# Kernel optimization log

Measured on AMD Instinct MI355X. Metric: run time of the kernel, lower is better.

The kernel has to match this reference:

```python
import jax, jax.numpy as jnp
import numpy as np

NUM_HEADS = 8
NUM_POINTS = 4


def _bilinear(img, xs, ys):
    """Bilinear sample with zero padding (grid_sample align_corners=False).
    img: [N, H, W, C]; xs, ys: [N, P] pixel-space coords. Returns [N, P, C]."""
    H, W = img.shape[1], img.shape[2]
    x0 = jnp.floor(xs)
    y0 = jnp.floor(ys)
    wx = xs - x0
    wy = ys - y0
    x0i = x0.astype(jnp.int32)
    y0i = y0.astype(jnp.int32)

    def g(ix, iy):
        valid = ((ix >= 0) & (ix < W) & (iy >= 0) & (iy < H)).astype(img.dtype)
        ixc = jnp.clip(ix, 0, W - 1)
        iyc = jnp.clip(iy, 0, H - 1)
        v = jax.vmap(lambda im, yy, xx: im[yy, xx])(img, iyc, ixc)  # [N,P,C]
        return v * valid[..., None]

    return (g(x0i, y0i) * ((1 - wx) * (1 - wy))[..., None]
            + g(x0i + 1, y0i) * (wx * (1 - wy))[..., None]
            + g(x0i, y0i + 1) * ((1 - wx) * wy)[..., None]
            + g(x0i + 1, y0i + 1) * (wx * wy)[..., None])


def setup_inputs() -> dict:
    key = jax.random.key(0)
    ks = jax.random.split(key, 10)
    BN, C, H, W = 12, 256, 40, 100
    nq = H * W
    hp = NUM_HEADS * NUM_POINTS
    s = 1.0 / np.sqrt(C).astype(np.float32)
    return {
        "img_feats": jax.random.normal(ks[0], (BN, C, H, W), jnp.float32),
        "warp_grid": jax.random.uniform(ks[1], (BN, H, W, 2), jnp.float32),
        "reference_points": jax.random.uniform(ks[2], (BN, nq, 1, 2), jnp.float32),
        "Wv": jax.random.normal(ks[3], (C, C), jnp.float32) * s,
        "bv": jnp.zeros((C,), jnp.float32),
        "Woff": jax.random.normal(ks[4], (C, hp * 2), jnp.float32) * 0.01,
        "boff": jax.random.normal(ks[5], (hp * 2,), jnp.float32) * 0.5,
        "Wattn": jax.random.normal(ks[6], (C, hp), jnp.float32) * 0.01,
        "battn": jnp.zeros((hp,), jnp.float32),
        "Wout": jax.random.normal(ks[7], (C, C), jnp.float32) * s,
        "bout": jnp.zeros((C,), jnp.float32),
    }


def reference(img_feats, warp_grid, reference_points,
              Wv, bv, Woff, boff, Wattn, battn, Wout, bout):
    BN, C, H, W = img_feats.shape
    heads, pts = NUM_HEADS, NUM_POINTS
    hd = C // heads
    nq = H * W

    feat = img_feats.transpose(0, 2, 3, 1)  # [BN, H, W, C]

    # BEVWarp: bilinear warp of image features at the projected grid ([0,1] normed)
    gx = warp_grid[..., 0].reshape(BN, -1) * W - 0.5
    gy = warp_grid[..., 1].reshape(BN, -1) * H - 0.5
    warped = _bilinear(feat, gx, gy)          # [BN, nq, C] -> value
    query = feat.reshape(BN, nq, C)           # flattened img feats -> query

    # MultiScaleDeformableAttention, num_levels=1
    v = (warped @ Wv + bv).reshape(BN, nq, heads, hd)
    off = (query @ Woff + boff).reshape(BN, nq, heads, pts, 2)
    attn = jax.nn.softmax((query @ Wattn + battn).reshape(BN, nq, heads, pts), axis=-1)

    norm = jnp.array([W, H], dtype=img_feats.dtype)
    loc = reference_points.reshape(BN, nq, 1, 1, 2) + off / norm  # [BN,nq,h,p,2]

    vh = v.transpose(0, 2, 1, 3).reshape(BN * heads, H, W, hd)
    lx = (loc[..., 0] * W - 0.5).transpose(0, 2, 1, 3).reshape(BN * heads, nq * pts)
    ly = (loc[..., 1] * H - 0.5).transpose(0, 2, 1, 3).reshape(BN * heads, nq * pts)
    sampled = _bilinear(vh, lx, ly).reshape(BN, heads, nq, pts, hd)

    agg = jnp.einsum('bhqpd,bqhp->bqhd', sampled, attn).reshape(BN, nq, C)
    out = agg @ Wout + bout + query  # output_proj + residual (dropout=0 at eval)
    return out.transpose(0, 2, 1).reshape(BN, C, H, W)
```

## Files before the change

### kernel.cpp

```cpp
#include <hip/hip_runtime.h>

#define DEVINL __device__ __forceinline__

typedef __attribute__((ext_vector_type(4))) float f32x4;
typedef __attribute__((ext_vector_type(8))) short short8;

constexpr int kBN = 12, kC = 256, kH = 40, kW = 100;
constexpr int kNQ = kH * kW;
constexpr int kM = kBN * kNQ;

DEVINL float bflo(uint p) { union { uint i; float f; } v; v.i = p << 16; return v.f; }
DEVINL float bfhi(uint p) { union { uint i; float f; } v; v.i = p & 0xffff0000u; return v.f; }
DEVINL ushort f2bf(float f) {
  union { float f; uint i; } v; v.f = f;
  uint i = v.i;
  return (ushort)((i + 0x7fffu + ((i >> 16) & 1u)) >> 16);
}
DEVINL uint pack2(float a, float b) { return (uint)f2bf(a) | ((uint)f2bf(b) << 16); }

DEVINL void mfma_bf16(f32x4& acc, short8 a, short8 b) {
  acc = __builtin_amdgcn_mfma_f32_16x16x32_bf16(a, b, acc, 0, 0, 0);
}

DEVINL void acc8(float* acc, uint4 d, float wv) {
  acc[0] += wv * bflo(d.x); acc[1] += wv * bfhi(d.x);
  acc[2] += wv * bflo(d.y); acc[3] += wv * bfhi(d.y);
  acc[4] += wv * bflo(d.z); acc[5] += wv * bfhi(d.z);
  acc[6] += wv * bflo(d.w); acc[7] += wv * bfhi(d.w);
}

__global__ __launch_bounds__(256) void k_wt(const float* __restrict__ W,
                                            ushort* __restrict__ WT, int K, int N) {
  int idx = blockIdx.x * 256 + threadIdx.x;
  if (idx >= K * N) return;
  int n = idx / K, k = idx - n * K;
  WT[idx] = f2bf(W[k * N + n]);
}

__global__ __launch_bounds__(256) void k_transpose(const float* __restrict__ img,
                                                   ushort* __restrict__ feat) {
  __shared__ ushort tile[64][66];
  int b = blockIdx.z, c0 = blockIdx.y * 64, q0 = blockIdx.x * 64;
  int t = threadIdx.x;
  int ql = t & 63, cl = t >> 6;
#pragma unroll
  for (int i = 0; i < 16; ++i) {
    int c = cl + i * 4, q = q0 + ql;
    float v = (q < kNQ) ? img[(size_t)(b * kC + c0 + c) * kNQ + q] : 0.f;
    tile[c][ql] = f2bf(v);
  }
  __syncthreads();
  int cc = t & 63, qr = t >> 6;
#pragma unroll
  for (int i = 0; i < 16; ++i) {
    int qlo = qr + i * 4, q = q0 + qlo;
    if (q < kNQ) feat[(size_t)(b * kNQ + q) * kC + c0 + cc] = tile[cc][qlo];
  }
}

__global__ __launch_bounds__(256) void k_warp(const ushort* __restrict__ feat,
                                              const float* __restrict__ grid,
                                              ushort* __restrict__ warped) {
  int orig = blockIdx.x;
  int n = (orig & 7) * 750 + (orig >> 3);
  int t = threadIdx.x;
  int ql = t >> 5, g = t & 31;
  int gq = n * 8 + ql;
  int b = gq / kNQ, q = gq - b * kNQ;
  float gx = grid[(size_t)gq * 2 + 0] * kW - 0.5f;
  float gy = grid[(size_t)gq * 2 + 1] * kH - 0.5f;
  float x0f = floorf(gx), y0f = floorf(gy);
  int x0 = (int)x0f, y0 = (int)y0f;
  float wx = gx - x0f, wy = gy - y0f;
  float acc[8];
#pragma unroll
  for (int i = 0; i < 8; ++i) acc[i] = 0.f;
  const ushort* fb = feat + (size_t)b * kNQ * kC + g * 8;
#pragma unroll
  for (int ty = 0; ty < 2; ++ty) {
    int iy = y0 + ty;
    if (iy < 0 || iy >= kH) continue;
    float wyv = ty ? wy : 1.f - wy;
#pragma unroll
    for (int tx = 0; tx < 2; ++tx) {
      int ix = x0 + tx;
      if (ix < 0 || ix >= kW) continue;
      float wv = wyv * (tx ? wx : 1.f - wx);
      uint4 d = *(const uint4*)(fb + (size_t)(iy * kW + ix) * kC);
      acc8(acc, d, wv);
    }
  }
  uint o[4] = {pack2(acc[0], acc[1]), pack2(acc[2], acc[3]),
               pack2(acc[4], acc[5]), pack2(acc[6], acc[7])};
  *(uint4*)(warped + (size_t)gq * kC + g * 8) = *(uint4*)o;
}

template <int EPI>
__global__ __launch_bounds__(256) void k_gemm256(const ushort* __restrict__ A,
                                                 const ushort* __restrict__ BT,
                                                 const float* __restrict__ bias,
                                                 ushort* __restrict__ Obf,
                                                 float* __restrict__ Ofp,
                                                 const float* __restrict__ resid) {
  extern __shared__ char smem[];
  ushort* As = (ushort*)smem;
  ushort* Bs = (ushort*)(smem + 2048);
  const int t = threadIdx.x, wave = t >> 6, lane = t & 63;
  const int l15 = lane & 15, l4 = lane >> 4;
  const int m0 = blockIdx.x * 32;
  const int n0w = wave * 64;
  f32x4 acc[2][4];
#pragma unroll
  for (int i = 0; i < 2; ++i)
#pragma unroll
    for (int j = 0; j < 4; ++j) acc[i][j] = (f32x4)0.f;

  for (int kk = 0; kk < 256; kk += 32) {
    if (t < 128) {
      int r = t >> 2, ch = t & 3;
      uint4 d = *(const uint4*)(A + (size_t)(m0 + r) * 256 + kk + ch * 8);
      *(uint4*)((char*)As + r * 64 + ((ch * 16) ^ ((r & 3) << 4))) = d;
    }
#pragma unroll
    for (int i = 0; i < 4; ++i) {
      int idx = t + i * 256;
      int r = idx >> 2, ch = idx & 3;
      uint4 d = *(const uint4*)(BT + (size_t)r * 256 + kk + ch * 8);
      *(uint4*)((char*)Bs + r * 64 + ((ch * 16) ^ ((r & 3) << 4))) = d;
    }
    __syncthreads();
    short8 a[2], bfr[4];
#pragma unroll
    for (int mf = 0; mf < 2; ++mf) {
      int r = mf * 16 + l15;
      a[mf] = *(const short8*)((char*)As + r * 64 + ((l4 * 16) ^ ((r & 3) << 4)));
    }
#pragma unroll
    for (int nf = 0; nf < 4; ++nf) {
      int r = n0w + nf * 16 + l15;
      bfr[nf] = *(const short8*)((char*)Bs + r * 64 + ((l4 * 16) ^ ((r & 3) << 4)));
    }
#pragma unroll
    for (int mf = 0; mf < 2; ++mf)
#pragma unroll
      for (int nf = 0; nf < 4; ++nf) mfma_bf16(acc[mf][nf], a[mf], bfr[nf]);
    __syncthreads();
  }

  if (EPI == 0) {
    int b = m0 / kNQ, q0 = m0 % kNQ;
#pragma unroll
    for (int mf = 0; mf < 2; ++mf)
#pragma unroll
      for (int nf = 0; nf < 4; ++nf) {
        int col = n0w + nf * 16 + l15;
        float bv = bias[col];
        int h = col >> 5, ch = col & 31;
#pragma unroll
        for (int j = 0; j < 4; ++j) {
          int q = q0 + mf * 16 + l4 * 4 + j;
          Obf[((size_t)(b * 8 + h) * kNQ + q) * 32 + ch] = f2bf(acc[mf][nf][j] + bv);
        }
      }
  } else {
    float* T = (float*)smem;
#pragma unroll
    for (int mf = 0; mf < 2; ++mf)
#pragma unroll
      for (int nf = 0; nf < 4; ++nf) {
        int col = n0w + nf * 16 + l15;
        float bv = bias[col];
#pragma unroll
        for (int j = 0; j < 4; ++j) {
          int rl = mf * 16 + l4 * 4 + j;
          T[col * 33 + rl] = acc[mf][nf][j] + bv;
        }
      }
    __syncthreads();
    int b = m0 / kNQ, q0 = m0 % kNQ;
    int qv = t & 31, cr = t >> 5;
#pragma unroll
    for (int i = 0; i < 32; ++i) {
      int c = cr + i * 8;
      size_t gi = (size_t)(b * kC + c) * kNQ + q0 + qv;
      Ofp[gi] = T[c * 33 + qv] + resid[gi];
    }
  }
}

__global__ __launch_bounds__(256) void k_offattn(const ushort* __restrict__ A,
                                                 const ushort* __restrict__ WoffT,
                                                 const ushort* __restrict__ WattnT,
                                                 const float* __restrict__ boff,
                                                 const float* __restrict__ battn,
                                                 const float* __restrict__ refp,
                                                 float4* __restrict__ samp) {
  __shared__ ushort As[32 * 32];
  __shared__ ushort Bs[96 * 32];
  __shared__ float T[32 * 100];
  const int t = threadIdx.x, wave = t >> 6, lane = t & 63;
  const int l15 = lane & 15, l4 = lane >> 4;
  const int m0 = blockIdx.x * 32;
  const int mf = wave & 1, nbase = (wave >> 1) * 48;
  f32x4 acc[3] = {(f32x4)0.f, (f32x4)0.f, (f32x4)0.f};

  for (int kk = 0; kk < 256; kk += 32) {
    if (t < 128) {
      int r = t >> 2, ch = t & 3;
      uint4 d = *(const uint4*)(A + (size_t)(m0 + r) * 256 + kk + ch * 8);
      *(uint4*)((char*)As + r * 64 + ((ch * 16) ^ ((r & 3) << 4))) = d;
    }
#pragma unroll
    for (int i = 0; i < 2; ++i) {
      int id = t + i * 256;
      if (id < 384) {
        int r = id >> 2, ch = id & 3;
        const ushort* src = (r < 64) ? (WoffT + (size_t)r * 256) : (WattnT + (size_t)(r - 64) * 256);
        uint4 d = *(const uint4*)(src + kk + ch * 8);
        *(uint4*)((char*)Bs + r * 64 + ((ch * 16) ^ ((r & 3) << 4))) = d;
      }
    }
    __syncthreads();
    short8 a;
    {
      int r = mf * 16 + l15;
      a = *(const short8*)((char*)As + r * 64 + ((l4 * 16) ^ ((r & 3) << 4)));
    }
#pragma unroll
    for (int nf = 0; nf < 3; ++nf) {
      int r = nbase + nf * 16 + l15;
      short8 bb = *(const short8*)((char*)Bs + r * 64 + ((l4 * 16) ^ ((r & 3) << 4)));
      mfma_bf16(acc[nf], a, bb);
    }
    __syncthreads();
  }
#pragma unroll
  for (int nf = 0; nf < 3; ++nf) {
    int col = nbase + nf * 16 + l15;
    float bv = (col < 64) ? boff[col] : battn[col - 64];
#pragma unroll
    for (int j = 0; j < 4; ++j) {
      int rl = mf * 16 + l4 * 4 + j;
      T[rl * 100 + col] = acc[nf][j] + bv;
    }
  }
  __syncthreads();
  int ql = t >> 3, h = t & 7;
  int b = m0 / kNQ, q = m0 % kNQ + ql;
  float refx = refp[(size_t)(b * kNQ + q) * 2 + 0] * kW - 0.5f;
  float refy = refp[(size_t)(b * kNQ + q) * 2 + 1] * kH - 0.5f;
  float sx[4], sy[4], lg[4];
#pragma unroll
  for (int p = 0; p < 4; ++p) {
    sx[p] = refx + T[ql * 100 + h * 8 + p * 2 + 0];
    sy[p] = refy + T[ql * 100 + h * 8 + p * 2 + 1];
    lg[p] = T[ql * 100 + 64 + h * 4 + p];
  }
  float mx = fmaxf(fmaxf(lg[0], lg[1]), fmaxf(lg[2], lg[3]));
  float e[4], s = 0.f;
#pragma unroll
  for (int p = 0; p < 4; ++p) { e[p] = __expf(lg[p] - mx); s += e[p]; }
  float inv = 1.f / s;
  float4* dst = samp + ((size_t)(b * 8 + h) * kNQ + q) * 4;
#pragma unroll
  for (int p = 0; p < 4; ++p) dst[p] = make_float4(sx[p], sy[p], e[p] * inv, 0.f);
}

__global__ __launch_bounds__(256) void k_sample(const ushort* __restrict__ v,
                                                const float4* __restrict__ samp,
                                                ushort* __restrict__ agg) {
  int orig = blockIdx.x;
  int n = (orig & 7) * 756 + (orig >> 3);
  int plane = n / 63, chunk = n - plane * 63;
  int t = threadIdx.x;
  int ql = t >> 2, g = t & 3;
  int q = chunk * 64 + ql;
  if (q >= kNQ) return;
  int b = plane >> 3, h = plane & 7;
  const ushort* pv = v + (size_t)plane * kNQ * 32 + g * 8;
  const int lane = t & 63, gbase = lane & ~3;

  float4 mys = samp[((size_t)plane * kNQ + q) * 4 + g];
  float acc[8];
#pragma unroll
  for (int i = 0; i < 8; ++i) acc[i] = 0.f;
#pragma unroll
  for (int p = 0; p < 4; ++p) {
    float sxp = __shfl(mys.x, gbase + p);
    float syp = __shfl(mys.y, gbase + p);
    float wp  = __shfl(mys.z, gbase + p);
    float x0f = floorf(sxp), y0f = floorf(syp);
    int x0 = (int)x0f, y0 = (int)y0f;
    float wx = sxp - x0f, wy = syp - y0f;
#pragma unroll
    for (int ty = 0; ty < 2; ++ty) {
      int iy = y0 + ty;
      if (iy < 0 || iy >= kH) continue;
      float wyv = ty ? wy : 1.f - wy;
#pragma unroll
      for (int tx = 0; tx < 2; ++tx) {
        int ix = x0 + tx;
        if (ix < 0 || ix >= kW) continue;
        float wv = wp * wyv * (tx ? wx : 1.f - wx);
        uint4 d = *(const uint4*)(pv + (size_t)(iy * kW + ix) * 32);
        acc8(acc, d, wv);
      }
    }
  }
  uint o[4] = {pack2(acc[0], acc[1]), pack2(acc[2], acc[3]),
               pack2(acc[4], acc[5]), pack2(acc[6], acc[7])};
  *(uint4*)(agg + ((size_t)b * kNQ + q) * kC + h * 32 + g * 8) = *(uint4*)o;
}

extern "C" void kernel_launch(void* const* d_in, const int* in_sizes, int n_in,
                              void* d_out, int out_size, void* d_ws, size_t ws_size,
                              hipStream_t stream) {
  const float* img   = (const float*)d_in[0];
  const float* grid  = (const float*)d_in[1];
  const float* refp  = (const float*)d_in[2];
  const float* Wv    = (const float*)d_in[3];
  const float* bv    = (const float*)d_in[4];
  const float* Woff  = (const float*)d_in[5];
  const float* boff  = (const float*)d_in[6];
  const float* Wattn = (const float*)d_in[7];
  const float* battn = (const float*)d_in[8];
  const float* Wout  = (const float*)d_in[9];
  const float* bout  = (const float*)d_in[10];
  float* out = (float*)d_out;

  char* ws = (char*)d_ws;
  const size_t SZ = (size_t)kM * kC * 2;
  ushort* feat   = (ushort*)(ws);
  ushort* warped = (ushort*)(ws + SZ);
  ushort* vbuf   = (ushort*)(ws + 2 * SZ);
  float4* samp   = (float4*)(ws + 3 * SZ);
  ushort* WvT    = (ushort*)(ws + 4 * SZ);
  ushort* WoffT  = (ushort*)(ws + 4 * SZ + 131072);
  ushort* WattnT = (ushort*)(ws + 4 * SZ + 131072 + 32768);
  ushort* WoutT  = (ushort*)(ws + 4 * SZ + 131072 + 32768 + 16384);
  ushort* aggb   = warped;

  k_wt<<<(65536 + 255) / 256, 256, 0, stream>>>(Wv, WvT, 256, 256);
  k_wt<<<(16384 + 255) / 256, 256, 0, stream>>>(Woff, WoffT, 256, 64);
  k_wt<<<(8192 + 255) / 256, 256, 0, stream>>>(Wattn, WattnT, 256, 32);
  k_wt<<<(65536 + 255) / 256, 256, 0, stream>>>(Wout, WoutT, 256, 256);

  k_transpose<<<dim3(63, 4, 12), 256, 0, stream>>>(img, feat);
  k_warp<<<6000, 256, 0, stream>>>(feat, grid, warped);
  k_gemm256<0><<<kM / 32, 256, 18432, stream>>>(warped, WvT, bv, vbuf, nullptr, nullptr);
  k_offattn<<<kM / 32, 256, 0, stream>>>(feat, WoffT, WattnT, boff, battn, refp, samp);
  k_sample<<<6048, 256, 0, stream>>>(vbuf, samp, aggb);
  k_gemm256<1><<<kM / 32, 256, 33792, stream>>>(aggb, WoutT, bout, nullptr, out, img);
}
```

Before: 141.8 us.

## Use 64-row per-batch GEMM tiles with direct global-to-LDS loads and vectorized epilogues

The three GEMM kernels now use 64-row M tiles indexed per batch plane (63 tiles per batch), which halves the number of blocks and doubles reuse of each loaded B tile. Operands are staged with global_load_lds (16-byte direct-to-LDS) using a new XOR swizzle, in place of register round-trips. The output-projection epilogue is rewritten to transpose per wave through LDS and write float4 residual-added output. The partial last tile per batch is handled by masking. Fewer blocks may reduce occupancy and latency hiding, and the per-batch split adds some wasted tile rows.

```diff
diff --git a/kernel.cpp b/kernel.cpp
--- a/kernel.cpp
+++ b/kernel.cpp
@@ -20,6 +20,12 @@
 
 DEVINL void mfma_bf16(f32x4& acc, short8 a, short8 b) {
   acc = __builtin_amdgcn_mfma_f32_16x16x32_bf16(a, b, acc, 0, 0, 0);
+}
+
+DEVINL void gload16(const ushort* g, char* lds) {
+  __builtin_amdgcn_global_load_lds(
+      (const __attribute__((address_space(1))) uint*)g,
+      (__attribute__((address_space(3))) uint*)lds, 16, 0, 0);
 }
 
 DEVINL void acc8(float* acc, uint4 d, float wv) {
@@ -66,7 +72,7 @@
   int t = threadIdx.x;
   int ql = t >> 5, g = t & 31;
   int gq = n * 8 + ql;
-  int b = gq / kNQ, q = gq - b * kNQ;
+  int b = gq / kNQ;
   float gx = grid[(size_t)gq * 2 + 0] * kW - 0.5f;
   float gy = grid[(size_t)gq * 2 + 1] * kH - 0.5f;
   float x0f = floorf(gx), y0f = floorf(gy);
@@ -103,87 +109,91 @@
                                                  float* __restrict__ Ofp,
                                                  const float* __restrict__ resid) {
   extern __shared__ char smem[];
-  ushort* As = (ushort*)smem;
-  ushort* Bs = (ushort*)(smem + 2048);
+  char* As = smem;
+  char* Bs = smem + 4096;
   const int t = threadIdx.x, wave = t >> 6, lane = t & 63;
   const int l15 = lane & 15, l4 = lane >> 4;
-  const int m0 = blockIdx.x * 32;
+  const int b = blockIdx.x / 63, mb = blockIdx.x % 63;
+  const int q0 = mb * 64;
+  const int nrows = (kNQ - q0 < 64) ? (kNQ - q0) : 64;
   const int n0w = wave * 64;
-  f32x4 acc[2][4];
-#pragma unroll
-  for (int i = 0; i < 2; ++i)
+  const int ra = t >> 2, ca = t & 3;
+  const int sca = ca ^ ((ra >> 1) & 3);
+  const ushort* gA = A + ((size_t)b * kNQ + q0 + ra) * 256 + sca * 8;
+  const ushort* gB = BT + (size_t)ra * 256 + sca * 8;
+  const bool doA = (ra < nrows);
+
+  f32x4 acc[4][4];
+#pragma unroll
+  for (int i = 0; i < 4; ++i)
 #pragma unroll
     for (int j = 0; j < 4; ++j) acc[i][j] = (f32x4)0.f;
 
   for (int kk = 0; kk < 256; kk += 32) {
-    if (t < 128) {
-      int r = t >> 2, ch = t & 3;
-      uint4 d = *(const uint4*)(A + (size_t)(m0 + r) * 256 + kk + ch * 8);
-      *(uint4*)((char*)As + r * 64 + ((ch * 16) ^ ((r & 3) << 4))) = d;
-    }
-#pragma unroll
-    for (int i = 0; i < 4; ++i) {
-      int idx = t + i * 256;
-      int r = idx >> 2, ch = idx & 3;
-      uint4 d = *(const uint4*)(BT + (size_t)r * 256 + kk + ch * 8);
-      *(uint4*)((char*)Bs + r * 64 + ((ch * 16) ^ ((r & 3) << 4))) = d;
-    }
+    if (doA) gload16(gA + kk, As + t * 16);
+#pragma unroll
+    for (int i = 0; i < 4; ++i)
+      gload16(gB + (size_t)i * 64 * 256 + kk, Bs + (i * 256 + t) * 16);
     __syncthreads();
-    short8 a[2], bfr[4];
-#pragma unroll
-    for (int mf = 0; mf < 2; ++mf) {
+    short8 af[4], bf[4];
+#pragma unroll
+    for (int mf = 0; mf < 4; ++mf) {
       int r = mf * 16 + l15;
-      a[mf] = *(const short8*)((char*)As + r * 64 + ((l4 * 16) ^ ((r & 3) << 4)));
+      int sl = l4 ^ ((r >> 1) & 3);
+      af[mf] = *(const short8*)(As + r * 64 + sl * 16);
     }
 #pragma unroll
     for (int nf = 0; nf < 4; ++nf) {
       int r = n0w + nf * 16 + l15;
-      bfr[nf] = *(const short8*)((char*)Bs + r * 64 + ((l4 * 16) ^ ((r & 3) << 4)));
-    }
-#pragma unroll
-    for (int mf = 0; mf < 2; ++mf)
-#pragma unroll
-      for (int nf = 0; nf < 4; ++nf) mfma_bf16(acc[mf][nf], a[mf], bfr[nf]);
+      int sl = l4 ^ ((r >> 1) & 3);
+      bf[nf] = *(const short8*)(Bs + r * 64 + sl * 16);
+    }
+#pragma unroll
+    for (int mf = 0; mf < 4; ++mf)
+#pragma unroll
+      for (int nf = 0; nf < 4; ++nf) mfma_bf16(acc[mf][nf], af[mf], bf[nf]);
     __syncthreads();
   }
 
   if (EPI == 0) {
-    int b = m0 / kNQ, q0 = m0 % kNQ;
-#pragma unroll
-    for (int mf = 0; mf < 2; ++mf)
+#pragma unroll
+    for (int mf = 0; mf < 4; ++mf) {
+      if (mf * 16 >= nrows) continue;
+      int q = q0 + mf * 16 + l4 * 4;
 #pragma unroll
       for (int nf = 0; nf < 4; ++nf) {
         int col = n0w + nf * 16 + l15;
         float bv = bias[col];
         int h = col >> 5, ch = col & 31;
-#pragma unroll
-        for (int j = 0; j < 4; ++j) {
-          int q = q0 + mf * 16 + l4 * 4 + j;
-          Obf[((size_t)(b * 8 + h) * kNQ + q) * 32 + ch] = f2bf(acc[mf][nf][j] + bv);
+        ushort* dst = Obf + (size_t)(b * 8 + h) * kNQ * 32 + ch;
+#pragma unroll
+        for (int j = 0; j < 4; ++j)
+          dst[(size_t)(q + j) * 32] = f2bf(acc[mf][nf][j] + bv);
+      }
+    }
+  } else {
+    float* Tw = (float*)(smem + wave * 4352);
+#pragma unroll
+    for (int nf = 0; nf < 4; ++nf) {
+      float bv = bias[n0w + nf * 16 + l15];
+#pragma unroll
+      for (int mf = 0; mf < 4; ++mf)
+#pragma unroll
+        for (int j = 0; j < 4; ++j)
+          Tw[l15 * 68 + mf * 16 + l4 * 4 + j] = acc[mf][nf][j] + bv;
+      int c = l15, hi = l4;
+      int rs = hi * 16;
+      if (rs < nrows) {
+        int col = n0w + nf * 16 + c;
+        size_t gi = ((size_t)b * kC + col) * kNQ + q0 + rs;
+#pragma unroll
+        for (int k = 0; k < 4; ++k) {
+          float4 tv = *(float4*)(&Tw[c * 68 + rs + k * 4]);
+          float4 rv = *(const float4*)(resid + gi + k * 4);
+          tv.x += rv.x; tv.y += rv.y; tv.z += rv.z; tv.w += rv.w;
+          *(float4*)(Ofp + gi + k * 4) = tv;
         }
       }
-  } else {
-    float* T = (float*)smem;
-#pragma unroll
-    for (int mf = 0; mf < 2; ++mf)
-#pragma unroll
-      for (int nf = 0; nf < 4; ++nf) {
-        int col = n0w + nf * 16 + l15;
-        float bv = bias[col];
-#pragma unroll
-        for (int j = 0; j < 4; ++j) {
-          int rl = mf * 16 + l4 * 4 + j;
-          T[col * 33 + rl] = acc[mf][nf][j] + bv;
-        }
-      }
-    __syncthreads();
-    int b = m0 / kNQ, q0 = m0 % kNQ;
-    int qv = t & 31, cr = t >> 5;
-#pragma unroll
-    for (int i = 0; i < 32; ++i) {
-      int c = cr + i * 8;
-      size_t gi = (size_t)(b * kC + c) * kNQ + q0 + qv;
-      Ofp[gi] = T[c * 33 + qv] + resid[gi];
     }
   }
 }
@@ -195,75 +205,92 @@
                                                  const float* __restrict__ battn,
                                                  const float* __restrict__ refp,
                                                  float4* __restrict__ samp) {
-  __shared__ ushort As[32 * 32];
-  __shared__ ushort Bs[96 * 32];
-  __shared__ float T[32 * 100];
+  extern __shared__ char smem[];
+  char* As = smem;
+  char* Bs = smem + 4096;
+  float* T = (float*)smem;
   const int t = threadIdx.x, wave = t >> 6, lane = t & 63;
   const int l15 = lane & 15, l4 = lane >> 4;
-  const int m0 = blockIdx.x * 32;
-  const int mf = wave & 1, nbase = (wave >> 1) * 48;
-  f32x4 acc[3] = {(f32x4)0.f, (f32x4)0.f, (f32x4)0.f};
+  const int b = blockIdx.x / 63, mb = blockIdx.x % 63;
+  const int q0 = mb * 64;
+  const int nrows = (kNQ - q0 < 64) ? (kNQ - q0) : 64;
+  const int wr = wave >> 1, wc = wave & 1;
+  const int ra = t >> 2, ca = t & 3;
+  const int sca = ca ^ ((ra >> 1) & 3);
+  const ushort* gA = A + ((size_t)b * kNQ + q0 + ra) * 256 + sca * 8;
+  const ushort* gB0 = WoffT + (size_t)ra * 256 + sca * 8;
+  const ushort* gB1 = WattnT + (size_t)ra * 256 + sca * 8;
+  const bool doA = (ra < nrows);
+
+  f32x4 acc[2][3];
+#pragma unroll
+  for (int i = 0; i < 2; ++i)
+#pragma unroll
+    for (int j = 0; j < 3; ++j) acc[i][j] = (f32x4)0.f;
 
   for (int kk = 0; kk < 256; kk += 32) {
-    if (t < 128) {
-      int r = t >> 2, ch = t & 3;
-      uint4 d = *(const uint4*)(A + (size_t)(m0 + r) * 256 + kk + ch * 8);
-      *(uint4*)((char*)As + r * 64 + ((ch * 16) ^ ((r & 3) << 4))) = d;
-    }
-#pragma unroll
-    for (int i = 0; i < 2; ++i) {
-      int id = t + i * 256;
-      if (id < 384) {
-        int r = id >> 2, ch = id & 3;
-        const ushort* src = (r < 64) ? (WoffT + (size_t)r * 256) : (WattnT + (size_t)(r - 64) * 256);
-        uint4 d = *(const uint4*)(src + kk + ch * 8);
-        *(uint4*)((char*)Bs + r * 64 + ((ch * 16) ^ ((r & 3) << 4))) = d;
-      }
-    }
+    if (doA) gload16(gA + kk, As + t * 16);
+    gload16(gB0 + kk, Bs + t * 16);
+    if (t < 128) gload16(gB1 + kk, Bs + (256 + t) * 16);
     __syncthreads();
-    short8 a;
-    {
-      int r = mf * 16 + l15;
-      a = *(const short8*)((char*)As + r * 64 + ((l4 * 16) ^ ((r & 3) << 4)));
+    short8 af[2], bf[3];
+#pragma unroll
+    for (int mf = 0; mf < 2; ++mf) {
+      int r = wr * 32 + mf * 16 + l15;
+      int sl = l4 ^ ((r >> 1) & 3);
+      af[mf] = *(const short8*)(As + r * 64 + sl * 16);
     }
 #pragma unroll
     for (int nf = 0; nf < 3; ++nf) {
-      int r = nbase + nf * 16 + l15;
-      short8 bb = *(const short8*)((char*)Bs + r * 64 + ((l4 * 16) ^ ((r & 3) << 4)));
-      mfma_bf16(acc[nf], a, bb);
-    }
+      int r = wc * 48 + nf * 16 + l15;
+      int sl = l4 ^ ((r >> 1) & 3);
+      bf[nf] = *(const short8*)(Bs + r * 64 + sl * 16);
+    }
+#pragma unroll
+    for (int mf = 0; mf < 2; ++mf)
+#pragma unroll
+      for (int nf = 0; nf < 3; ++nf) mfma_bf16(acc[mf][nf], af[mf], bf[nf]);
     __syncthreads();
   }
+
 #pragma unroll
   for (int nf = 0; nf < 3; ++nf) {
-    int col = nbase + nf * 16 + l15;
+    int col = wc * 48 + nf * 16 + l15;
     float bv = (col < 64) ? boff[col] : battn[col - 64];
 #pragma unroll
-    for (int j = 0; j < 4; ++j) {
-      int rl = mf * 16 + l4 * 4 + j;
-      T[rl * 100 + col] = acc[nf][j] + bv;
-    }
+    for (int mf = 0; mf < 2; ++mf)
+#pragma unroll
+      for (int j = 0; j < 4; ++j) {
+        int row = wr * 32 + mf * 16 + l4 * 4 + j;
+        T[row * 101 + col] = acc[mf][nf][j] + bv;
+      }
   }
   __syncthreads();
-  int ql = t >> 3, h = t & 7;
-  int b = m0 / kNQ, q = m0 % kNQ + ql;
-  float refx = refp[(size_t)(b * kNQ + q) * 2 + 0] * kW - 0.5f;
-  float refy = refp[(size_t)(b * kNQ + q) * 2 + 1] * kH - 0.5f;
-  float sx[4], sy[4], lg[4];
-#pragma unroll
-  for (int p = 0; p < 4; ++p) {
-    sx[p] = refx + T[ql * 100 + h * 8 + p * 2 + 0];
-    sy[p] = refy + T[ql * 100 + h * 8 + p * 2 + 1];
-    lg[p] = T[ql * 100 + 64 + h * 4 + p];
-  }
-  float mx = fmaxf(fmaxf(lg[0], lg[1]), fmaxf(lg[2], lg[3]));
-  float e[4], s = 0.f;
-#pragma unroll
-  for (int p = 0; p < 4; ++p) { e[p] = __expf(lg[p] - mx); s += e[p]; }
-  float inv = 1.f / s;
-  float4* dst = samp + ((size_t)(b * 8 + h) * kNQ + q) * 4;
-#pragma unroll
-  for (int p = 0; p < 4; ++p) dst[p] = make_float4(sx[p], sy[p], e[p] * inv, 0.f);
+  int row = t >> 2;
+  if (row < nrows) {
+    int q = q0 + row;
+    float refx = refp[((size_t)b * kNQ + q) * 2 + 0] * kW - 0.5f;
+    float refy = refp[((size_t)b * kNQ + q) * 2 + 1] * kH - 0.5f;
+#pragma unroll
+    for (int hi2 = 0; hi2 < 2; ++hi2) {
+      int h = (t & 3) + hi2 * 4;
+      float sx[4], sy[4], lg[4];
+#pragma unroll
+      for (int p = 0; p < 4; ++p) {
+        sx[p] = refx + T[row * 101 + h * 8 + p * 2 + 0];
+        sy[p] = refy + T[row * 101 + h * 8 + p * 2 + 1];
+        lg[p] = T[row * 101 + 64 + h * 4 + p];
+      }
+      float mx = fmaxf(fmaxf(lg[0], lg[1]), fmaxf(lg[2], lg[3]));
+      float e[4], s = 0.f;
+#pragma unroll
+      for (int p = 0; p < 4; ++p) { e[p] = __expf(lg[p] - mx); s += e[p]; }
+      float inv = 1.f / s;
+      float4* dst = samp + ((size_t)(b * 8 + h) * kNQ + q) * 4;
+#pragma unroll
+      for (int p = 0; p < 4; ++p) dst[p] = make_float4(sx[p], sy[p], e[p] * inv, 0.f);
+    }
+  }
 }
 
 __global__ __launch_bounds__(256) void k_sample(const ushort* __restrict__ v,
@@ -347,8 +374,8 @@
 
   k_transpose<<<dim3(63, 4, 12), 256, 0, stream>>>(img, feat);
   k_warp<<<6000, 256, 0, stream>>>(feat, grid, warped);
-  k_gemm256<0><<<kM / 32, 256, 18432, stream>>>(warped, WvT, bv, vbuf, nullptr, nullptr);
-  k_offattn<<<kM / 32, 256, 0, stream>>>(feat, WoffT, WattnT, boff, battn, refp, samp);
+  k_gemm256<0><<<756, 256, 20480, stream>>>(warped, WvT, bv, vbuf, nullptr, nullptr);
+  k_offattn<<<756, 256, 25856, stream>>>(feat, WoffT, WattnT, boff, battn, refp, samp);
   k_sample<<<6048, 256, 0, stream>>>(vbuf, samp, aggb);
-  k_gemm256<1><<<kM / 32, 256, 33792, stream>>>(aggb, WoutT, bout, nullptr, out, img);
-}
+  k_gemm256<1><<<756, 256, 20480, stream>>>(aggb, WoutT, bout, nullptr, out, img);
+}
```

After: 135.1 us. -4.8%, faster.
